# Kernel tuning notes

Measured on AMD Instinct MI355X. Metric: run time of the kernel, lower is better.

The kernel has to match this reference:

```python
import jax, jax.numpy as jnp
import numpy as np
import math

L, D, H, FF = 6, 512, 8, 2048
B, S = 8, 1024
EPS = 1e-5


def sin_pos_embedding(num_embeddings, dim, padding_idx=0):
    half = dim // 2
    freq = jnp.exp(jnp.arange(half, dtype=jnp.float32) * (-math.log(10000.0) / (half - 1)))
    ang = jnp.arange(num_embeddings, dtype=jnp.float32)[:, None] * freq[None, :]
    emb = jnp.concatenate([jnp.sin(ang), jnp.cos(ang)], axis=1)
    return emb.at[padding_idx].set(0.0)


def layer_norm(x, g, b):
    mu = jnp.mean(x, axis=-1, keepdims=True)
    var = jnp.mean(jnp.square(x - mu), axis=-1, keepdims=True)
    return (x - mu) * jax.lax.rsqrt(var + EPS) * g + b


def setup_inputs() -> dict:
    key = jax.random.key(0)
    ks = jax.random.split(key, 16)
    s = 0.02
    inp = {
        'x': jax.random.normal(ks[0], (B, S, D), jnp.float32),
        'char_ids': jax.random.randint(ks[1], (B, S), 0, 10000, jnp.int64) if jax.config.read('jax_enable_x64') else jax.random.randint(ks[1], (B, S), 0, 10000, jnp.int32),
        'seq_len': jnp.full((B,), S, jnp.int32),
        'mask': jnp.ones((B, S), jnp.int32),
        'Wqkv': jax.random.normal(ks[2], (L, D, 3 * D), jnp.float32) * s,
        'Wfc': jax.random.normal(ks[3], (L, D, D), jnp.float32) * s,
        'bfc': jnp.zeros((L, D), jnp.float32),
        'ln1_g': jnp.ones((L, D), jnp.float32), 'ln1_b': jnp.zeros((L, D), jnp.float32),
        'ln2_g': jnp.ones((L, D), jnp.float32), 'ln2_b': jnp.zeros((L, D), jnp.float32),
        'W1': jax.random.normal(ks[4], (L, D, FF), jnp.float32) * s,
        'b1': jnp.zeros((L, FF), jnp.float32),
        'W2': jax.random.normal(ks[5], (L, FF, D), jnp.float32) * s,
        'b2': jnp.zeros((L, D), jnp.float32),
    }
    return inp


def reference(x, char_ids, seq_len, mask, Wqkv, Wfc, bfc, ln1_g, ln1_b, ln2_g, ln2_b, W1, b1, W2, b2):
    # sinusoidal positional embedding computed from mask positions (padding_idx=0)
    valid = (mask != 0).astype(jnp.int32)
    positions = jnp.cumsum(valid, axis=1) * valid  # [B,S], pads -> 0
    table = sin_pos_embedding(S + 2, D)  # max_pos = padding_idx+1+S
    x = x + table[positions]

    key_mask = (mask == 0)[:, None, None, :]  # [B,1,1,S]
    dh = D // H

    for l in range(L):
        residual = x
        qkv = jnp.einsum('bsd,de->bse', x, Wqkv[l])  # [B,S,3D]
        q, k, v = jnp.split(qkv, 3, axis=-1)
        q = q.reshape(B, S, H, dh).transpose(0, 2, 1, 3)  # [B,H,S,dh]
        k = k.reshape(B, S, H, dh).transpose(0, 2, 1, 3)
        v = v.reshape(B, S, H, dh).transpose(0, 2, 1, 3)
        attn = jnp.einsum('bhqd,bhkd->bhqk', q, k)  # scale=1 (scale=False)
        attn = jnp.where(key_mask, -jnp.inf, attn)
        attn = jax.nn.softmax(attn, axis=-1)
        o = jnp.einsum('bhqk,bhkd->bhqd', attn, v)
        o = o.transpose(0, 2, 1, 3).reshape(B, S, D)
        o = jnp.einsum('bsd,de->bse', o, Wfc[l]) + bfc[l]
        x = layer_norm(o + residual, ln1_g[l], ln1_b[l])
        residual = x
        h = jax.nn.relu(jnp.einsum('bsd,df->bsf', x, W1[l]) + b1[l])
        h = jnp.einsum('bsf,fd->bsd', h, W2[l]) + b2[l]
        x = layer_norm(residual + h, ln2_g[l], ln2_b[l])
    return x
```

## Files before the change

### kernel.cpp

```cpp
#include <hip/hip_runtime.h>
#include <math.h>

#define LAYERS 6
#define DMODEL 512
#define NHEAD 8
#define DHEAD 64
#define FFDIM 2048
#define BATCH 8
#define SEQ 1024
#define ROWS (BATCH * SEQ)
#define EPS 1e-5f

typedef __attribute__((ext_vector_type(8))) short bf16x8;
typedef __attribute__((ext_vector_type(4))) float f32x4;
typedef __attribute__((ext_vector_type(16))) float f32x16;

__device__ inline short f2bf(float f) {
    union { float f; unsigned u; } v; v.f = f;
    unsigned r = (v.u + 0x7FFFu + ((v.u >> 16) & 1u)) >> 16;
    return (short)r;
}

#define GLOAD_LDS16(g, l)                                                      \
    __builtin_amdgcn_global_load_lds(                                          \
        (__attribute__((address_space(1))) void*)(g),                          \
        (__attribute__((address_space(3))) void*)(l), 16, 0, 0)

__global__ void wtrans_kernel(const float* __restrict__ src, short* __restrict__ dst,
                              int K, int N) {
    __shared__ float t[32][33];
    const size_t mofs = (size_t)blockIdx.z * K * N;
    src += mofs; dst += mofs;
    int n0 = blockIdx.x * 32, k0 = blockIdx.y * 32;
    int tx = threadIdx.x, ty = threadIdx.y;
#pragma unroll
    for (int i = 0; i < 4; ++i)
        t[ty + 8 * i][tx] = src[(size_t)(k0 + ty + 8 * i) * N + n0 + tx];
    __syncthreads();
#pragma unroll
    for (int i = 0; i < 4; ++i)
        dst[(size_t)(n0 + ty + 8 * i) * K + k0 + tx] = f2bf(t[tx][ty + 8 * i]);
}

__global__ void pos_scan_kernel(const int* __restrict__ mask, int* __restrict__ pos) {
    __shared__ int sm[SEQ];
    int b = blockIdx.x;
    int t = threadIdx.x;
    int v = (mask[b * SEQ + t] != 0) ? 1 : 0;
    sm[t] = v;
    __syncthreads();
    for (int off = 1; off < SEQ; off <<= 1) {
        int add = (t >= off) ? sm[t - off] : 0;
        __syncthreads();
        sm[t] += add;
        __syncthreads();
    }
    pos[b * SEQ + t] = sm[t] * v;
}

__global__ void add_pos_kernel(const float* __restrict__ xin, const int* __restrict__ pos,
                               float* __restrict__ xout, short* __restrict__ xb) {
    int bs = blockIdx.x;
    int t = threadIdx.x;
    int p = pos[bs];
    int d0 = t * 4;
    const float C = -logf(10000.0f) * (1.0f / 255.0f);
    float4 xv = *(const float4*)(xin + (size_t)bs * DMODEL + d0);
    float e[4];
#pragma unroll
    for (int j = 0; j < 4; ++j) {
        int d = d0 + j;
        if (p == 0) {
            e[j] = 0.0f;
        } else {
            int dd = (d < 256) ? d : d - 256;
            float freq = expf((float)dd * C);
            float ang = (float)p * freq;
            e[j] = (d < 256) ? sinf(ang) : cosf(ang);
        }
    }
    float4 ov;
    ov.x = xv.x + e[0]; ov.y = xv.y + e[1]; ov.z = xv.z + e[2]; ov.w = xv.w + e[3];
    *(float4*)(xout + (size_t)bs * DMODEL + d0) = ov;
    short4 sb;
    sb.x = f2bf(ov.x); sb.y = f2bf(ov.y); sb.z = f2bf(ov.z); sb.w = f2bf(ov.w);
    *(short4*)(xb + (size_t)bs * DMODEL + d0) = sb;
}


template <bool OUTBF16, bool BIAS, bool RELU>
__global__ __launch_bounds__(256) void gemm_bf16_kernel(const short* __restrict__ A,
                                                        const short* __restrict__ BT,
                                                        const float* __restrict__ bias,
                                                        void* __restrict__ Cv,
                                                        int M, int N, int K) {
    __shared__ __attribute__((aligned(16))) short Asm[2][128 * 32];
    __shared__ __attribute__((aligned(16))) short Bsm[2][128 * 32];
    const int tid = threadIdx.x;
    const int w = tid >> 6;
    const int lane = tid & 63;
    const int quad = lane >> 4;
    const int lr = lane & 15;
    const int m0 = blockIdx.y * 128;
    const int n0 = blockIdx.x * 128;
    const int wm = (w >> 1) * 64;
    const int wn = (w & 1) * 64;

    const int segr = lane >> 2;
    const int segk = (((lane & 3) - (lane >> 3)) & 3) * 8;
    const int sA0 = w * 2, sA1 = w * 2 + 1;
    const short* gA0 = A + (size_t)(m0 + sA0 * 16 + segr) * K + segk;
    const short* gA1 = A + (size_t)(m0 + sA1 * 16 + segr) * K + segk;
    const short* gB0 = BT + (size_t)(n0 + sA0 * 16 + segr) * K + segk;
    const short* gB1 = BT + (size_t)(n0 + sA1 * 16 + segr) * K + segk;
    const int lofs0 = sA0 * 512 + lane * 8;
    const int lofs1 = sA1 * 512 + lane * 8;
    const int gp = ((quad + (lr >> 1)) & 3) * 8;

    f32x4 acc[4][4];
#pragma unroll
    for (int i = 0; i < 4; ++i)
#pragma unroll
        for (int j = 0; j < 4; ++j) { acc[i][j][0] = 0.f; acc[i][j][1] = 0.f; acc[i][j][2] = 0.f; acc[i][j][3] = 0.f; }

    GLOAD_LDS16(gA0, &Asm[0][lofs0]);
    GLOAD_LDS16(gA1, &Asm[0][lofs1]);
    GLOAD_LDS16(gB0, &Bsm[0][lofs0]);
    GLOAD_LDS16(gB1, &Bsm[0][lofs1]);

    const int nk = K >> 5;
    for (int i = 0; i < nk; ++i) {
        __syncthreads();
        if (i + 1 < nk) {
            const int k1 = (i + 1) * 32;
            const int nb = (i + 1) & 1;
            GLOAD_LDS16(gA0 + k1, &Asm[nb][lofs0]);
            GLOAD_LDS16(gA1 + k1, &Asm[nb][lofs1]);
            GLOAD_LDS16(gB0 + k1, &Bsm[nb][lofs0]);
            GLOAD_LDS16(gB1 + k1, &Bsm[nb][lofs1]);
        }
        const int cur = i & 1;
        bf16x8 af[4], bfr[4];
#pragma unroll
        for (int mt = 0; mt < 4; ++mt)
            af[mt] = *(const bf16x8*)&Asm[cur][(wm + mt * 16 + lr) * 32 + gp];
#pragma unroll
        for (int nt = 0; nt < 4; ++nt)
            bfr[nt] = *(const bf16x8*)&Bsm[cur][(wn + nt * 16 + lr) * 32 + gp];
#pragma unroll
        for (int mt = 0; mt < 4; ++mt)
#pragma unroll
            for (int nt = 0; nt < 4; ++nt)
                acc[mt][nt] = __builtin_amdgcn_mfma_f32_16x16x32_bf16(af[mt], bfr[nt], acc[mt][nt], 0, 0, 0);
    }

    float bv[4];
    if (BIAS) {
#pragma unroll
        for (int nt = 0; nt < 4; ++nt) bv[nt] = bias[n0 + wn + nt * 16 + lr];
    }
#pragma unroll
    for (int mt = 0; mt < 4; ++mt)
#pragma unroll
        for (int nt = 0; nt < 4; ++nt)
#pragma unroll
            for (int r = 0; r < 4; ++r) {
                float v = acc[mt][nt][r];
                if (BIAS) v += bv[nt];
                if (RELU) v = fmaxf(v, 0.f);
                int row = m0 + wm + mt * 16 + quad * 4 + r;
                int col = n0 + wn + nt * 16 + lr;
                if (OUTBF16)
                    ((short*)Cv)[(size_t)row * N + col] = f2bf(v);
                else
                    ((float*)Cv)[(size_t)row * N + col] = v;
            }
}

template <bool OUTBF16, bool BIAS, bool RELU>
__global__ __launch_bounds__(256) void gemm_bf16_m64_kernel(const short* __restrict__ A,
                                                            const short* __restrict__ BT,
                                                            const float* __restrict__ bias,
                                                            void* __restrict__ Cv,
                                                            int M, int N, int K) {
    __shared__ __attribute__((aligned(16))) short Asm[2][64 * 32];
    __shared__ __attribute__((aligned(16))) short Bsm[2][128 * 32];
    const int tid = threadIdx.x;
    const int w = tid >> 6;
    const int lane = tid & 63;
    const int quad = lane >> 4;
    const int lr = lane & 15;
    const int m0 = blockIdx.y * 64;
    const int n0 = blockIdx.x * 128;
    const int wm = (w >> 1) * 32;
    const int wn = (w & 1) * 64;

    const int segr = lane >> 2;
    const int segk = (((lane & 3) - (lane >> 3)) & 3) * 8;
    const short* gA  = A + (size_t)(m0 + w * 16 + segr) * K + segk;
    const short* gB0 = BT + (size_t)(n0 + (2 * w) * 16 + segr) * K + segk;
    const short* gB1 = BT + (size_t)(n0 + (2 * w + 1) * 16 + segr) * K + segk;
    const int lA  = w * 512 + lane * 8;
    const int lB0 = (2 * w) * 512 + lane * 8;
    const int lB1 = (2 * w + 1) * 512 + lane * 8;
    const int gp = ((quad + (lr >> 1)) & 3) * 8;

    f32x4 acc[2][4];
#pragma unroll
    for (int i = 0; i < 2; ++i)
#pragma unroll
        for (int j = 0; j < 4; ++j) { acc[i][j][0] = 0.f; acc[i][j][1] = 0.f; acc[i][j][2] = 0.f; acc[i][j][3] = 0.f; }

    GLOAD_LDS16(gA, &Asm[0][lA]);
    GLOAD_LDS16(gB0, &Bsm[0][lB0]);
    GLOAD_LDS16(gB1, &Bsm[0][lB1]);

    const int nk = K >> 5;
    for (int i = 0; i < nk; ++i) {
        __syncthreads();
        if (i + 1 < nk) {
            const int k1 = (i + 1) * 32;
            const int nb = (i + 1) & 1;
            GLOAD_LDS16(gA + k1, &Asm[nb][lA]);
            GLOAD_LDS16(gB0 + k1, &Bsm[nb][lB0]);
            GLOAD_LDS16(gB1 + k1, &Bsm[nb][lB1]);
        }
        const int cur = i & 1;
        bf16x8 af[2], bfr[4];
#pragma unroll
        for (int mt = 0; mt < 2; ++mt)
            af[mt] = *(const bf16x8*)&Asm[cur][(wm + mt * 16 + lr) * 32 + gp];
#pragma unroll
        for (int nt = 0; nt < 4; ++nt)
            bfr[nt] = *(const bf16x8*)&Bsm[cur][(wn + nt * 16 + lr) * 32 + gp];
#pragma unroll
        for (int mt = 0; mt < 2; ++mt)
#pragma unroll
            for (int nt = 0; nt < 4; ++nt)
                acc[mt][nt] = __builtin_amdgcn_mfma_f32_16x16x32_bf16(af[mt], bfr[nt], acc[mt][nt], 0, 0, 0);
    }

    float bv[4];
    if (BIAS) {
#pragma unroll
        for (int nt = 0; nt < 4; ++nt) bv[nt] = bias[n0 + wn + nt * 16 + lr];
    }
#pragma unroll
    for (int mt = 0; mt < 2; ++mt)
#pragma unroll
        for (int nt = 0; nt < 4; ++nt)
#pragma unroll
            for (int r = 0; r < 4; ++r) {
                float v = acc[mt][nt][r];
                if (BIAS) v += bv[nt];
                if (RELU) v = fmaxf(v, 0.f);
                int row = m0 + wm + mt * 16 + quad * 4 + r;
                int col = n0 + wn + nt * 16 + lr;
                if (OUTBF16)
                    ((short*)Cv)[(size_t)row * N + col] = f2bf(v);
                else
                    ((float*)Cv)[(size_t)row * N + col] = v;
            }
}

#define QTILE 256
__global__ __launch_bounds__(512, 2) void attn_mfma_kernel(const short* __restrict__ qkv,
                                                           const int* __restrict__ mask,
                                                           short* __restrict__ o) {
    __shared__ __attribute__((aligned(16))) short Ks[2][64][72];
    __shared__ __attribute__((aligned(16))) short Vt[2][64][72];
    __shared__ __attribute__((aligned(16))) float Msf[2][64];

    const int qt = blockIdx.x;
    const int bh = blockIdx.y;
    const int b = bh >> 3, h = bh & 7;
    const int tid = threadIdx.x;
    const int w = tid >> 6;
    const int lane = tid & 63;
    const int c31 = lane & 31;
    const int hi = lane >> 5;
    const size_t seqrow = (size_t)b * SEQ;

    bf16x8 qf[4];
#pragma unroll
    for (int ks = 0; ks < 4; ++ks)
        qf[ks] = *(const bf16x8*)(qkv +
            (seqrow + qt * QTILE + w * 32 + c31) * (3 * DMODEL)
            + h * DHEAD + ks * 16 + hi * 8);

    const bool isK = (tid < 256);
    const int st = isK ? tid : tid - 256;
    const int kkey = st >> 2;
    const int kg = (st & 3) * 8;
    const int vkp = st & 31;
    const int vdg = st >> 5;
    const short* gK = qkv + (seqrow + kkey) * (3 * DMODEL) + DMODEL + h * DHEAD + kg;
    const short* gV = qkv + (seqrow + 2 * vkp) * (3 * DMODEL) + 2 * DMODEL + h * DHEAD + vdg * 8;

    bf16x8 r0, r1;
    int mreg = 0;

    {
        if (isK) {
            r0 = *(const bf16x8*)(gK);
            r1 = *(const bf16x8*)(gK + 32);
        } else {
            r0 = *(const bf16x8*)(gV);
            r1 = *(const bf16x8*)(gV + 3 * DMODEL);
        }
        if (tid < 64) mreg = mask[seqrow + tid];
        if (isK) {
            *(bf16x8*)&Ks[0][kkey][kg] = r0;
            *(bf16x8*)&Ks[0][kkey][kg + 32] = r1;
        } else {
#pragma unroll
            for (int i = 0; i < 8; ++i) {
                short2 p; p.x = r0[i]; p.y = r1[i];
                *(short2*)&Vt[0][vdg * 8 + i][vkp * 2] = p;
            }
        }
        if (tid < 64) Msf[0][tid] = mreg ? 1.0f : 0.0f;
    }
    __syncthreads();

    f32x16 O0, O1;
    float rs = 0.f;
#pragma unroll
    for (int i = 0; i < 16; ++i) { O0[i] = 0.f; O1[i] = 0.f; }

    for (int kt = 0; kt < 16; ++kt) {
        const int cur = kt & 1;
        {
            const size_t ofs = (size_t)((kt + 1) & 15) * 64 * (3 * DMODEL);
            if (isK) {
                r0 = *(const bf16x8*)(gK + ofs);
                r1 = *(const bf16x8*)(gK + ofs + 32);
            } else {
                r0 = *(const bf16x8*)(gV + ofs);
                r1 = *(const bf16x8*)(gV + ofs + 3 * DMODEL);
            }
            if (tid < 64) mreg = mask[seqrow + ((kt + 1) & 15) * 64 + tid];
        }

        f32x16 S0, S1;
#pragma unroll
        for (int i = 0; i < 16; ++i) { S0[i] = 0.f; S1[i] = 0.f; }
#pragma unroll
        for (int ks = 0; ks < 4; ++ks) {
            bf16x8 k0 = *(const bf16x8*)&Ks[cur][c31][ks * 16 + hi * 8];
            bf16x8 k1 = *(const bf16x8*)&Ks[cur][32 + c31][ks * 16 + hi * 8];
            S0 = __builtin_amdgcn_mfma_f32_32x32x16_bf16(k0, qf[ks], S0, 0, 0, 0);
            S1 = __builtin_amdgcn_mfma_f32_32x32x16_bf16(k1, qf[ks], S1, 0, 0, 0);
        }

        unsigned pkd[2][8];
#pragma unroll
        for (int g = 0; g < 4; ++g) {
            f32x4 m0 = *(const f32x4*)&Msf[cur][g * 8 + hi * 4];
            f32x4 m1 = *(const f32x4*)&Msf[cur][32 + g * 8 + hi * 4];
            float p0[4], p1[4];
#pragma unroll
            for (int j = 0; j < 4; ++j) {
                p0[j] = __expf(S0[g * 4 + j] - 8.0f) * m0[j];
                p1[j] = __expf(S1[g * 4 + j] - 8.0f) * m1[j];
                rs += p0[j] + p1[j];
            }
            asm("v_cvt_pk_bf16_f32 %0, %1, %2" : "=v"(pkd[0][g * 2])     : "v"(p0[0]), "v"(p0[1]));
            asm("v_cvt_pk_bf16_f32 %0, %1, %2" : "=v"(pkd[0][g * 2 + 1]) : "v"(p0[2]), "v"(p0[3]));
            asm("v_cvt_pk_bf16_f32 %0, %1, %2" : "=v"(pkd[1][g * 2])     : "v"(p1[0]), "v"(p1[1]));
            asm("v_cvt_pk_bf16_f32 %0, %1, %2" : "=v"(pkd[1][g * 2 + 1]) : "v"(p1[2]), "v"(p1[3]));
        }

#pragma unroll
        for (int ks = 0; ks < 4; ++ks) {
            const int k2 = ks >> 1;
            const int i0 = (ks & 1) * 4;
            unsigned c0a = pkd[k2][i0 + 0], c0b = pkd[k2][i0 + 1];
            unsigned c1a = pkd[k2][i0 + 2], c1b = pkd[k2][i0 + 3];
            unsigned x1a = (unsigned)__shfl_xor((int)c1a, 32);
            unsigned x1b = (unsigned)__shfl_xor((int)c1b, 32);
            unsigned x0a = (unsigned)__shfl_xor((int)c0a, 32);
            unsigned x0b = (unsigned)__shfl_xor((int)c0b, 32);
            union { unsigned u[4]; bf16x8 v; } pb;
            pb.u[0] = hi ? x1a : c0a;
            pb.u[1] = hi ? x1b : c0b;
            pb.u[2] = hi ? c1a : x0a;
            pb.u[3] = hi ? c1b : x0b;
            bf16x8 v0 = *(const bf16x8*)&Vt[cur][c31][ks * 16 + hi * 8];
            bf16x8 v1 = *(const bf16x8*)&Vt[cur][32 + c31][ks * 16 + hi * 8];
            O0 = __builtin_amdgcn_mfma_f32_32x32x16_bf16(pb.v, v0, O0, 0, 0, 0);
            O1 = __builtin_amdgcn_mfma_f32_32x32x16_bf16(pb.v, v1, O1, 0, 0, 0);
        }

        {
            const int nb = cur ^ 1;
            if (isK) {
                *(bf16x8*)&Ks[nb][kkey][kg] = r0;
                *(bf16x8*)&Ks[nb][kkey][kg + 32] = r1;
            } else {
#pragma unroll
                for (int i = 0; i < 8; ++i) {
                    short2 p; p.x = r0[i]; p.y = r1[i];
                    *(short2*)&Vt[nb][vdg * 8 + i][vkp * 2] = p;
                }
            }
            if (tid < 64) Msf[nb][tid] = mreg ? 1.0f : 0.0f;
        }
        __syncthreads();
    }

    rs += __shfl_xor(rs, 32);

#pragma unroll
    for (int r = 0; r < 16; ++r) {
        const int qr = (r & 3) + 8 * (r >> 2) + 4 * hi;
        const float inv = 1.0f / __shfl(rs, qr);
        const int row = qt * QTILE + w * 32 + qr;
        o[(seqrow + row) * DMODEL + h * DHEAD + c31]      = f2bf(O0[r] * inv);
        o[(seqrow + row) * DMODEL + h * DHEAD + 32 + c31] = f2bf(O1[r] * inv);
    }
}

__global__ __launch_bounds__(64) void ln_kernel(const float* __restrict__ tmp,
                                                float* __restrict__ x,
                                                short* __restrict__ xb,
                                                const float* __restrict__ g,
                                                const float* __restrict__ bta) {
    const int row = blockIdx.x;
    const int t = threadIdx.x;
    const size_t base = (size_t)row * DMODEL + t * 8;
    float4 x0 = *(const float4*)(x + base);
    float4 x1 = *(const float4*)(x + base + 4);
    float4 t0 = *(const float4*)(tmp + base);
    float4 t1 = *(const float4*)(tmp + base + 4);
    float v[8];
    v[0] = x0.x + t0.x; v[1] = x0.y + t0.y; v[2] = x0.z + t0.z; v[3] = x0.w + t0.w;
    v[4] = x1.x + t1.x; v[5] = x1.y + t1.y; v[6] = x1.z + t1.z; v[7] = x1.w + t1.w;
    float s = 0.f, sq = 0.f;
#pragma unroll
    for (int i = 0; i < 8; ++i) { s += v[i]; sq += v[i] * v[i]; }
#pragma unroll
    for (int off = 1; off < 64; off <<= 1) {
        s += __shfl_xor(s, off);
        sq += __shfl_xor(sq, off);
    }
    float mu = s * (1.0f / DMODEL);
    float var = sq * (1.0f / DMODEL) - mu * mu;
    float r = rsqrtf(var + EPS);
    float4 g0 = *(const float4*)(g + t * 8);
    float4 g1 = *(const float4*)(g + t * 8 + 4);
    float4 b0 = *(const float4*)(bta + t * 8);
    float4 b1 = *(const float4*)(bta + t * 8 + 4);
    float ov[8];
    ov[0] = (v[0] - mu) * r * g0.x + b0.x;
    ov[1] = (v[1] - mu) * r * g0.y + b0.y;
    ov[2] = (v[2] - mu) * r * g0.z + b0.z;
    ov[3] = (v[3] - mu) * r * g0.w + b0.w;
    ov[4] = (v[4] - mu) * r * g1.x + b1.x;
    ov[5] = (v[5] - mu) * r * g1.y + b1.y;
    ov[6] = (v[6] - mu) * r * g1.z + b1.z;
    ov[7] = (v[7] - mu) * r * g1.w + b1.w;
    *(float4*)(x + base) = *(float4*)&ov[0];
    *(float4*)(x + base + 4) = *(float4*)&ov[4];
    bf16x8 ob;
#pragma unroll
    for (int i = 0; i < 8; ++i) ob[i] = f2bf(ov[i]);
    *(bf16x8*)(xb + base) = ob;
}

extern "C" void kernel_launch(void* const* d_in, const int* in_sizes, int n_in,
                              void* d_out, int out_size, void* d_ws, size_t ws_size,
                              hipStream_t stream) {
    const float* x_in  = (const float*)d_in[0];
    const int*   mask  = (const int*)d_in[3];
    const float* Wqkv  = (const float*)d_in[4];
    const float* Wfc   = (const float*)d_in[5];
    const float* bfc   = (const float*)d_in[6];
    const float* ln1_g = (const float*)d_in[7];
    const float* ln1_b = (const float*)d_in[8];
    const float* ln2_g = (const float*)d_in[9];
    const float* ln2_b = (const float*)d_in[10];
    const float* W1    = (const float*)d_in[11];
    const float* b1    = (const float*)d_in[12];
    const float* W2    = (const float*)d_in[13];
    const float* b2    = (const float*)d_in[14];

    float* x = (float*)d_out;

    char* ws = (char*)d_ws;
    size_t ofs = 0;
    int*   pos   = (int*)ws;                 ofs += 65536;
    float* tmp   = (float*)(ws + ofs);       ofs += (size_t)ROWS * DMODEL * 4;
    short* xb    = (short*)(ws + ofs);       ofs += (size_t)ROWS * DMODEL * 2;
    short* qkvb  = (short*)(ws + ofs);
    short* hb    = (short*)(ws + ofs);
    ofs += (size_t)ROWS * 3 * DMODEL * 2;
    short* obuf  = (short*)(ws + ofs);       ofs += (size_t)ROWS * DMODEL * 2;
    short* WqkvT = (short*)(ws + ofs);       ofs += (size_t)LAYERS * DMODEL * 3 * DMODEL * 2;
    short* WfcT  = (short*)(ws + ofs);       ofs += (size_t)LAYERS * DMODEL * DMODEL * 2;
    short* W1T   = (short*)(ws + ofs);       ofs += (size_t)LAYERS * DMODEL * FFDIM * 2;
    short* W2T   = (short*)(ws + ofs);       ofs += (size_t)LAYERS * FFDIM * DMODEL * 2;

    wtrans_kernel<<<dim3(3 * DMODEL / 32, DMODEL / 32, LAYERS), dim3(32, 8), 0, stream>>>(
        Wqkv, WqkvT, DMODEL, 3 * DMODEL);
    wtrans_kernel<<<dim3(DMODEL / 32, DMODEL / 32, LAYERS), dim3(32, 8), 0, stream>>>(
        Wfc, WfcT, DMODEL, DMODEL);
    wtrans_kernel<<<dim3(FFDIM / 32, DMODEL / 32, LAYERS), dim3(32, 8), 0, stream>>>(
        W1, W1T, DMODEL, FFDIM);
    wtrans_kernel<<<dim3(DMODEL / 32, FFDIM / 32, LAYERS), dim3(32, 8), 0, stream>>>(
        W2, W2T, FFDIM, DMODEL);

    pos_scan_kernel<<<BATCH, SEQ, 0, stream>>>(mask, pos);
    add_pos_kernel<<<ROWS, 128, 0, stream>>>(x_in, pos, x, xb);

    for (int l = 0; l < LAYERS; ++l) {
        const short* wqkvT_l = WqkvT + (size_t)l * DMODEL * 3 * DMODEL;
        const short* wfcT_l  = WfcT + (size_t)l * DMODEL * DMODEL;
        const short* w1T_l   = W1T + (size_t)l * DMODEL * FFDIM;
        const short* w2T_l   = W2T + (size_t)l * FFDIM * DMODEL;
        const float* bfc_l   = bfc + (size_t)l * DMODEL;
        const float* b1_l    = b1 + (size_t)l * FFDIM;
        const float* b2_l    = b2 + (size_t)l * DMODEL;

        gemm_bf16_kernel<true, false, false><<<dim3(3 * DMODEL / 128, ROWS / 128), 256, 0, stream>>>(
            xb, wqkvT_l, nullptr, qkvb, ROWS, 3 * DMODEL, DMODEL);
        attn_mfma_kernel<<<dim3(SEQ / QTILE, BATCH * NHEAD), 512, 0, stream>>>(qkvb, mask, obuf);
        gemm_bf16_m64_kernel<false, true, false><<<dim3(DMODEL / 128, ROWS / 64), 256, 0, stream>>>(
            obuf, wfcT_l, bfc_l, tmp, ROWS, DMODEL, DMODEL);
        ln_kernel<<<ROWS, 64, 0, stream>>>(tmp, x, xb, ln1_g + (size_t)l * DMODEL,
                                           ln1_b + (size_t)l * DMODEL);
        gemm_bf16_kernel<true, true, true><<<dim3(FFDIM / 128, ROWS / 128), 256, 0, stream>>>(
            xb, w1T_l, b1_l, hb, ROWS, FFDIM, DMODEL);
        gemm_bf16_m64_kernel<false, true, false><<<dim3(DMODEL / 128, ROWS / 64), 256, 0, stream>>>(
            hb, w2T_l, b2_l, tmp, ROWS, DMODEL, FFDIM);
        ln_kernel<<<ROWS, 64, 0, stream>>>(tmp, x, xb, ln2_g + (size_t)l * DMODEL,
                                           ln2_b + (size_t)l * DMODEL);
    }
}
```

Baseline: 1.091 ms.

## Emit pre-transposed V from QKV GEMM and stream K/V from global in attention

The QKV GEMM now writes the V part as bf16 into a per-head, key-tiled transposed buffer (reusing the tmp workspace). The attention kernel drops its LDS double-buffering and barriers and instead loads K and the pre-transposed V straight from global memory into registers, unrolling the 16 key tiles with software prefetch. The full mask is staged once into LDS. Separately, the m64 GEMM processes a 64-wide K step per barrier instead of 32. This removes the in-kernel V transpose and most attention syncs, at the cost of heavier global/L2 traffic per wave and more register pressure.

```diff
diff --git a/kernel.cpp b/kernel.cpp
--- a/kernel.cpp
+++ b/kernel.cpp
@@ -88,11 +88,12 @@
 }
 
 
-template <bool OUTBF16, bool BIAS, bool RELU>
+template <bool OUTBF16, bool BIAS, bool RELU, bool SPLITV>
 __global__ __launch_bounds__(256) void gemm_bf16_kernel(const short* __restrict__ A,
                                                         const short* __restrict__ BT,
                                                         const float* __restrict__ bias,
                                                         void* __restrict__ Cv,
+                                                        short* __restrict__ Vt,
                                                         int M, int N, int K) {
     __shared__ __attribute__((aligned(16))) short Asm[2][128 * 32];
     __shared__ __attribute__((aligned(16))) short Bsm[2][128 * 32];
@@ -154,6 +155,25 @@
                 acc[mt][nt] = __builtin_amdgcn_mfma_f32_16x16x32_bf16(af[mt], bfr[nt], acc[mt][nt], 0, 0, 0);
     }
 
+    if (SPLITV && n0 >= 2 * DMODEL) {
+#pragma unroll
+        for (int mt = 0; mt < 4; ++mt)
+#pragma unroll
+            for (int nt = 0; nt < 4; ++nt) {
+                const int col = n0 + wn + nt * 16 + lr - 2 * DMODEL;
+                const int hh = col >> 6, dd = col & 63;
+                const int row = m0 + wm + mt * 16 + quad * 4;
+                const int bb = row >> 10, key = row & 1023;
+                short4 s4;
+                s4.x = f2bf(acc[mt][nt][0]);
+                s4.y = f2bf(acc[mt][nt][1]);
+                s4.z = f2bf(acc[mt][nt][2]);
+                s4.w = f2bf(acc[mt][nt][3]);
+                *(short4*)&Vt[(((size_t)(bb * 8 + hh) * 16 + (key >> 6)) * 64 + dd) * 64 + (key & 63)] = s4;
+            }
+        return;
+    }
+
     float bv[4];
     if (BIAS) {
 #pragma unroll
@@ -183,8 +203,8 @@
                                                             const float* __restrict__ bias,
                                                             void* __restrict__ Cv,
                                                             int M, int N, int K) {
-    __shared__ __attribute__((aligned(16))) short Asm[2][64 * 32];
-    __shared__ __attribute__((aligned(16))) short Bsm[2][128 * 32];
+    __shared__ __attribute__((aligned(16))) short Asm[2][2][64 * 32];
+    __shared__ __attribute__((aligned(16))) short Bsm[2][2][128 * 32];
     const int tid = threadIdx.x;
     const int w = tid >> 6;
     const int lane = tid & 63;
@@ -211,33 +231,42 @@
 #pragma unroll
         for (int j = 0; j < 4; ++j) { acc[i][j][0] = 0.f; acc[i][j][1] = 0.f; acc[i][j][2] = 0.f; acc[i][j][3] = 0.f; }
 
-    GLOAD_LDS16(gA, &Asm[0][lA]);
-    GLOAD_LDS16(gB0, &Bsm[0][lB0]);
-    GLOAD_LDS16(gB1, &Bsm[0][lB1]);
-
-    const int nk = K >> 5;
+#pragma unroll
+    for (int kh = 0; kh < 2; ++kh) {
+        GLOAD_LDS16(gA + kh * 32, &Asm[0][kh][lA]);
+        GLOAD_LDS16(gB0 + kh * 32, &Bsm[0][kh][lB0]);
+        GLOAD_LDS16(gB1 + kh * 32, &Bsm[0][kh][lB1]);
+    }
+
+    const int nk = K >> 6;
     for (int i = 0; i < nk; ++i) {
         __syncthreads();
         if (i + 1 < nk) {
-            const int k1 = (i + 1) * 32;
+            const int k1 = (i + 1) * 64;
             const int nb = (i + 1) & 1;
-            GLOAD_LDS16(gA + k1, &Asm[nb][lA]);
-            GLOAD_LDS16(gB0 + k1, &Bsm[nb][lB0]);
-            GLOAD_LDS16(gB1 + k1, &Bsm[nb][lB1]);
+#pragma unroll
+            for (int kh = 0; kh < 2; ++kh) {
+                GLOAD_LDS16(gA + k1 + kh * 32, &Asm[nb][kh][lA]);
+                GLOAD_LDS16(gB0 + k1 + kh * 32, &Bsm[nb][kh][lB0]);
+                GLOAD_LDS16(gB1 + k1 + kh * 32, &Bsm[nb][kh][lB1]);
+            }
         }
         const int cur = i & 1;
-        bf16x8 af[2], bfr[4];
-#pragma unroll
-        for (int mt = 0; mt < 2; ++mt)
-            af[mt] = *(const bf16x8*)&Asm[cur][(wm + mt * 16 + lr) * 32 + gp];
-#pragma unroll
-        for (int nt = 0; nt < 4; ++nt)
-            bfr[nt] = *(const bf16x8*)&Bsm[cur][(wn + nt * 16 + lr) * 32 + gp];
-#pragma unroll
-        for (int mt = 0; mt < 2; ++mt)
+#pragma unroll
+        for (int kh = 0; kh < 2; ++kh) {
+            bf16x8 af[2], bfr[4];
+#pragma unroll
+            for (int mt = 0; mt < 2; ++mt)
+                af[mt] = *(const bf16x8*)&Asm[cur][kh][(wm + mt * 16 + lr) * 32 + gp];
 #pragma unroll
             for (int nt = 0; nt < 4; ++nt)
-                acc[mt][nt] = __builtin_amdgcn_mfma_f32_16x16x32_bf16(af[mt], bfr[nt], acc[mt][nt], 0, 0, 0);
+                bfr[nt] = *(const bf16x8*)&Bsm[cur][kh][(wn + nt * 16 + lr) * 32 + gp];
+#pragma unroll
+            for (int mt = 0; mt < 2; ++mt)
+#pragma unroll
+                for (int nt = 0; nt < 4; ++nt)
+                    acc[mt][nt] = __builtin_amdgcn_mfma_f32_16x16x32_bf16(af[mt], bfr[nt], acc[mt][nt], 0, 0, 0);
+        }
     }
 
     float bv[4];
@@ -264,12 +293,70 @@
 }
 
 #define QTILE 256
+
+#define LDK(KR, KT) do {                                                       \
+    _Pragma("unroll")                                                          \
+    for (int ks_ = 0; ks_ < 4; ++ks_) {                                        \
+        KR[2 * ks_]     = *(const bf16x8*)(Kp + (size_t)(KT) * 98304 + ks_ * 16);            \
+        KR[2 * ks_ + 1] = *(const bf16x8*)(Kp + (size_t)(KT) * 98304 + 49152 + ks_ * 16);    \
+    } } while (0)
+
+#define LDV(VR, KT) do {                                                       \
+    _Pragma("unroll")                                                          \
+    for (int ks_ = 0; ks_ < 4; ++ks_) {                                        \
+        VR[2 * ks_]     = *(const bf16x8*)(Vp + (KT) * 4096 + ks_ * 16);         \
+        VR[2 * ks_ + 1] = *(const bf16x8*)(Vp + (KT) * 4096 + 2048 + ks_ * 16);  \
+    } } while (0)
+
+#define ATILE(KC, VV, KT) do {                                                 \
+    f32x16 S0, S1;                                                             \
+    _Pragma("unroll") for (int i_ = 0; i_ < 16; ++i_) { S0[i_] = 0.f; S1[i_] = 0.f; } \
+    _Pragma("unroll")                                                          \
+    for (int ks_ = 0; ks_ < 4; ++ks_) {                                        \
+        S0 = __builtin_amdgcn_mfma_f32_32x32x16_bf16(KC[2 * ks_], qf[ks_], S0, 0, 0, 0);     \
+        S1 = __builtin_amdgcn_mfma_f32_32x32x16_bf16(KC[2 * ks_ + 1], qf[ks_], S1, 0, 0, 0); \
+    }                                                                          \
+    unsigned pkd[2][8];                                                        \
+    _Pragma("unroll")                                                          \
+    for (int g_ = 0; g_ < 4; ++g_) {                                           \
+        f32x4 m0 = *(const f32x4*)&Msk[(KT) * 64 + g_ * 8 + hi * 4];           \
+        f32x4 m1 = *(const f32x4*)&Msk[(KT) * 64 + 32 + g_ * 8 + hi * 4];      \
+        float p0[4], p1[4];                                                    \
+        _Pragma("unroll")                                                      \
+        for (int j_ = 0; j_ < 4; ++j_) {                                       \
+            p0[j_] = __expf(S0[g_ * 4 + j_] - 8.0f) * m0[j_];                  \
+            p1[j_] = __expf(S1[g_ * 4 + j_] - 8.0f) * m1[j_];                  \
+            rs += p0[j_] + p1[j_];                                             \
+        }                                                                      \
+        asm("v_cvt_pk_bf16_f32 %0, %1, %2" : "=v"(pkd[0][g_ * 2])     : "v"(p0[0]), "v"(p0[1])); \
+        asm("v_cvt_pk_bf16_f32 %0, %1, %2" : "=v"(pkd[0][g_ * 2 + 1]) : "v"(p0[2]), "v"(p0[3])); \
+        asm("v_cvt_pk_bf16_f32 %0, %1, %2" : "=v"(pkd[1][g_ * 2])     : "v"(p1[0]), "v"(p1[1])); \
+        asm("v_cvt_pk_bf16_f32 %0, %1, %2" : "=v"(pkd[1][g_ * 2 + 1]) : "v"(p1[2]), "v"(p1[3])); \
+    }                                                                          \
+    _Pragma("unroll")                                                          \
+    for (int ks_ = 0; ks_ < 4; ++ks_) {                                        \
+        const int k2_ = ks_ >> 1;                                              \
+        const int i0_ = (ks_ & 1) * 4;                                         \
+        unsigned c0a = pkd[k2_][i0_ + 0], c0b = pkd[k2_][i0_ + 1];             \
+        unsigned c1a = pkd[k2_][i0_ + 2], c1b = pkd[k2_][i0_ + 3];             \
+        unsigned x1a = (unsigned)__shfl_xor((int)c1a, 32);                     \
+        unsigned x1b = (unsigned)__shfl_xor((int)c1b, 32);                     \
+        unsigned x0a = (unsigned)__shfl_xor((int)c0a, 32);                     \
+        unsigned x0b = (unsigned)__shfl_xor((int)c0b, 32);                     \
+        union { unsigned u[4]; bf16x8 v; } pb;                                 \
+        pb.u[0] = hi ? x1a : c0a;                                              \
+        pb.u[1] = hi ? x1b : c0b;                                              \
+        pb.u[2] = hi ? c1a : x0a;                                              \
+        pb.u[3] = hi ? c1b : x0b;                                              \
+        O0 = __builtin_amdgcn_mfma_f32_32x32x16_bf16(pb.v, VV[2 * ks_], O0, 0, 0, 0);     \
+        O1 = __builtin_amdgcn_mfma_f32_32x32x16_bf16(pb.v, VV[2 * ks_ + 1], O1, 0, 0, 0); \
+    } } while (0)
+
 __global__ __launch_bounds__(512, 2) void attn_mfma_kernel(const short* __restrict__ qkv,
+                                                           const short* __restrict__ Vtb,
                                                            const int* __restrict__ mask,
                                                            short* __restrict__ o) {
-    __shared__ __attribute__((aligned(16))) short Ks[2][64][72];
-    __shared__ __attribute__((aligned(16))) short Vt[2][64][72];
-    __shared__ __attribute__((aligned(16))) float Msf[2][64];
+    __shared__ float Msk[SEQ];
 
     const int qt = blockIdx.x;
     const int bh = blockIdx.y;
@@ -281,6 +368,9 @@
     const int hi = lane >> 5;
     const size_t seqrow = (size_t)b * SEQ;
 
+    Msk[tid] = mask[seqrow + tid] ? 1.0f : 0.0f;
+    Msk[tid + 512] = mask[seqrow + 512 + tid] ? 1.0f : 0.0f;
+
     bf16x8 qf[4];
 #pragma unroll
     for (int ks = 0; ks < 4; ++ks)
@@ -288,39 +378,9 @@
             (seqrow + qt * QTILE + w * 32 + c31) * (3 * DMODEL)
             + h * DHEAD + ks * 16 + hi * 8);
 
-    const bool isK = (tid < 256);
-    const int st = isK ? tid : tid - 256;
-    const int kkey = st >> 2;
-    const int kg = (st & 3) * 8;
-    const int vkp = st & 31;
-    const int vdg = st >> 5;
-    const short* gK = qkv + (seqrow + kkey) * (3 * DMODEL) + DMODEL + h * DHEAD + kg;
-    const short* gV = qkv + (seqrow + 2 * vkp) * (3 * DMODEL) + 2 * DMODEL + h * DHEAD + vdg * 8;
-
-    bf16x8 r0, r1;
-    int mreg = 0;
-
-    {
-        if (isK) {
-            r0 = *(const bf16x8*)(gK);
-            r1 = *(const bf16x8*)(gK + 32);
-        } else {
-            r0 = *(const bf16x8*)(gV);
-            r1 = *(const bf16x8*)(gV + 3 * DMODEL);
-        }
-        if (tid < 64) mreg = mask[seqrow + tid];
-        if (isK) {
-            *(bf16x8*)&Ks[0][kkey][kg] = r0;
-            *(bf16x8*)&Ks[0][kkey][kg + 32] = r1;
-        } else {
-#pragma unroll
-            for (int i = 0; i < 8; ++i) {
-                short2 p; p.x = r0[i]; p.y = r1[i];
-                *(short2*)&Vt[0][vdg * 8 + i][vkp * 2] = p;
-            }
-        }
-        if (tid < 64) Msf[0][tid] = mreg ? 1.0f : 0.0f;
-    }
+    const short* Kp = qkv + (seqrow + c31) * (3 * DMODEL) + DMODEL + h * DHEAD + hi * 8;
+    const short* Vp = Vtb + (size_t)bh * 65536 + c31 * 64 + hi * 8;
+
     __syncthreads();
 
     f32x16 O0, O1;
@@ -328,85 +388,16 @@
 #pragma unroll
     for (int i = 0; i < 16; ++i) { O0[i] = 0.f; O1[i] = 0.f; }
 
-    for (int kt = 0; kt < 16; ++kt) {
-        const int cur = kt & 1;
-        {
-            const size_t ofs = (size_t)((kt + 1) & 15) * 64 * (3 * DMODEL);
-            if (isK) {
-                r0 = *(const bf16x8*)(gK + ofs);
-                r1 = *(const bf16x8*)(gK + ofs + 32);
-            } else {
-                r0 = *(const bf16x8*)(gV + ofs);
-                r1 = *(const bf16x8*)(gV + ofs + 3 * DMODEL);
-            }
-            if (tid < 64) mreg = mask[seqrow + ((kt + 1) & 15) * 64 + tid];
-        }
-
-        f32x16 S0, S1;
-#pragma unroll
-        for (int i = 0; i < 16; ++i) { S0[i] = 0.f; S1[i] = 0.f; }
-#pragma unroll
-        for (int ks = 0; ks < 4; ++ks) {
-            bf16x8 k0 = *(const bf16x8*)&Ks[cur][c31][ks * 16 + hi * 8];
-            bf16x8 k1 = *(const bf16x8*)&Ks[cur][32 + c31][ks * 16 + hi * 8];
-            S0 = __builtin_amdgcn_mfma_f32_32x32x16_bf16(k0, qf[ks], S0, 0, 0, 0);
-            S1 = __builtin_amdgcn_mfma_f32_32x32x16_bf16(k1, qf[ks], S1, 0, 0, 0);
-        }
-
-        unsigned pkd[2][8];
-#pragma unroll
-        for (int g = 0; g < 4; ++g) {
-            f32x4 m0 = *(const f32x4*)&Msf[cur][g * 8 + hi * 4];
-            f32x4 m1 = *(const f32x4*)&Msf[cur][32 + g * 8 + hi * 4];
-            float p0[4], p1[4];
-#pragma unroll
-            for (int j = 0; j < 4; ++j) {
-                p0[j] = __expf(S0[g * 4 + j] - 8.0f) * m0[j];
-                p1[j] = __expf(S1[g * 4 + j] - 8.0f) * m1[j];
-                rs += p0[j] + p1[j];
-            }
-            asm("v_cvt_pk_bf16_f32 %0, %1, %2" : "=v"(pkd[0][g * 2])     : "v"(p0[0]), "v"(p0[1]));
-            asm("v_cvt_pk_bf16_f32 %0, %1, %2" : "=v"(pkd[0][g * 2 + 1]) : "v"(p0[2]), "v"(p0[3]));
-            asm("v_cvt_pk_bf16_f32 %0, %1, %2" : "=v"(pkd[1][g * 2])     : "v"(p1[0]), "v"(p1[1]));
-            asm("v_cvt_pk_bf16_f32 %0, %1, %2" : "=v"(pkd[1][g * 2 + 1]) : "v"(p1[2]), "v"(p1[3]));
-        }
-
-#pragma unroll
-        for (int ks = 0; ks < 4; ++ks) {
-            const int k2 = ks >> 1;
-            const int i0 = (ks & 1) * 4;
-            unsigned c0a = pkd[k2][i0 + 0], c0b = pkd[k2][i0 + 1];
-            unsigned c1a = pkd[k2][i0 + 2], c1b = pkd[k2][i0 + 3];
-            unsigned x1a = (unsigned)__shfl_xor((int)c1a, 32);
-            unsigned x1b = (unsigned)__shfl_xor((int)c1b, 32);
-            unsigned x0a = (unsigned)__shfl_xor((int)c0a, 32);
-            unsigned x0b = (unsigned)__shfl_xor((int)c0b, 32);
-            union { unsigned u[4]; bf16x8 v; } pb;
-            pb.u[0] = hi ? x1a : c0a;
-            pb.u[1] = hi ? x1b : c0b;
-            pb.u[2] = hi ? c1a : x0a;
-            pb.u[3] = hi ? c1b : x0b;
-            bf16x8 v0 = *(const bf16x8*)&Vt[cur][c31][ks * 16 + hi * 8];
-            bf16x8 v1 = *(const bf16x8*)&Vt[cur][32 + c31][ks * 16 + hi * 8];
-            O0 = __builtin_amdgcn_mfma_f32_32x32x16_bf16(pb.v, v0, O0, 0, 0, 0);
-            O1 = __builtin_amdgcn_mfma_f32_32x32x16_bf16(pb.v, v1, O1, 0, 0, 0);
-        }
-
-        {
-            const int nb = cur ^ 1;
-            if (isK) {
-                *(bf16x8*)&Ks[nb][kkey][kg] = r0;
-                *(bf16x8*)&Ks[nb][kkey][kg + 32] = r1;
-            } else {
-#pragma unroll
-                for (int i = 0; i < 8; ++i) {
-                    short2 p; p.x = r0[i]; p.y = r1[i];
-                    *(short2*)&Vt[nb][vdg * 8 + i][vkp * 2] = p;
-                }
-            }
-            if (tid < 64) Msf[nb][tid] = mreg ? 1.0f : 0.0f;
-        }
-        __syncthreads();
+    bf16x8 kA[8], kB[8], vv[8];
+    LDK(kA, 0);
+#pragma unroll
+    for (int t2 = 0; t2 < 8; ++t2) {
+        LDK(kB, 2 * t2 + 1);
+        LDV(vv, 2 * t2);
+        ATILE(kA, vv, 2 * t2);
+        if (t2 < 7) LDK(kA, 2 * t2 + 2);
+        LDV(vv, 2 * t2 + 1);
+        ATILE(kB, vv, 2 * t2 + 1);
     }
 
     rs += __shfl_xor(rs, 32);
@@ -500,6 +491,7 @@
     short* WfcT  = (short*)(ws + ofs);       ofs += (size_t)LAYERS * DMODEL * DMODEL * 2;
     short* W1T   = (short*)(ws + ofs);       ofs += (size_t)LAYERS * DMODEL * FFDIM * 2;
     short* W2T   = (short*)(ws + ofs);       ofs += (size_t)LAYERS * FFDIM * DMODEL * 2;
+    short* Vtb   = (short*)tmp;
 
     wtrans_kernel<<<dim3(3 * DMODEL / 32, DMODEL / 32, LAYERS), dim3(32, 8), 0, stream>>>(
         Wqkv, WqkvT, DMODEL, 3 * DMODEL);
@@ -522,15 +514,15 @@
         const float* b1_l    = b1 + (size_t)l * FFDIM;
         const float* b2_l    = b2 + (size_t)l * DMODEL;
 
-        gemm_bf16_kernel<true, false, false><<<dim3(3 * DMODEL / 128, ROWS / 128), 256, 0, stream>>>(
-            xb, wqkvT_l, nullptr, qkvb, ROWS, 3 * DMODEL, DMODEL);
-        attn_mfma_kernel<<<dim3(SEQ / QTILE, BATCH * NHEAD), 512, 0, stream>>>(qkvb, mask, obuf);
+        gemm_bf16_kernel<true, false, false, true><<<dim3(3 * DMODEL / 128, ROWS / 128), 256, 0, stream>>>(
+            xb, wqkvT_l, nullptr, qkvb, Vtb, ROWS, 3 * DMODEL, DMODEL);
+        attn_mfma_kernel<<<dim3(SEQ / QTILE, BATCH * NHEAD), 512, 0, stream>>>(qkvb, Vtb, mask, obuf);
         gemm_bf16_m64_kernel<false, true, false><<<dim3(DMODEL / 128, ROWS / 64), 256, 0, stream>>>(
             obuf, wfcT_l, bfc_l, tmp, ROWS, DMODEL, DMODEL);
         ln_kernel<<<ROWS, 64, 0, stream>>>(tmp, x, xb, ln1_g + (size_t)l * DMODEL,
                                            ln1_b + (size_t)l * DMODEL);
-        gemm_bf16_kernel<true, true, true><<<dim3(FFDIM / 128, ROWS / 128), 256, 0, stream>>>(
-            xb, w1T_l, b1_l, hb, ROWS, FFDIM, DMODEL);
+        gemm_bf16_kernel<true, true, true, false><<<dim3(FFDIM / 128, ROWS / 128), 256, 0, stream>>>(
+            xb, w1T_l, b1_l, hb, nullptr, ROWS, FFDIM, DMODEL);
         gemm_bf16_m64_kernel<false, true, false><<<dim3(DMODEL / 128, ROWS / 64), 256, 0, stream>>>(
             hb, w2T_l, b2_l, tmp, ROWS, DMODEL, FFDIM);
         ln_kernel<<<ROWS, 64, 0, stream>>>(tmp, x, xb, ln2_g + (size_t)l * DMODEL,
```

Measured after the change: 2.572 ms. 2.36x slower.
